# Kernel optimization log

Measured on AMD Instinct MI355X. Metric: run time of the kernel, lower is better.

The kernel has to match this reference:

```python
import jax, jax.numpy as jnp
import numpy as np

HID = 4096
H = 32
DK = 128
DV = 128
QKV = H * DK * 2 + H * DV  # 12288
EPS = 1e-06


def setup_inputs() -> dict:
    key = jax.random.key(0)
    ks = jax.random.split(key, 12)
    s = 0.02
    return {
        "hidden_states": jax.random.normal(ks[0], (1, 1, HID), jnp.float32),
        "delta_state": jax.random.normal(ks[1], (1, H, DV, DK), jnp.float32) * 0.1,
        "conv_state": jax.random.normal(ks[2], (1, QKV, 1, 3), jnp.float32),
        "W_qkv": jax.random.normal(ks[3], (QKV, HID), jnp.float32) * s,
        "W_z": jax.random.normal(ks[4], (H * DV, HID), jnp.float32) * s,
        "W_a": jax.random.normal(ks[5], (H, HID), jnp.float32) * s,
        "W_b": jax.random.normal(ks[6], (H, HID), jnp.float32) * s,
        "W_out": jax.random.normal(ks[7], (HID, H * DV), jnp.float32) * s,
        "conv_w": jax.random.normal(ks[8], (1, QKV, 1, 4), jnp.float32) * 0.01,
        "A_log": jnp.zeros((H,), jnp.float32),
        "dt_bias": jnp.zeros((H,), jnp.float32),
        "rms_weight": jnp.ones((DV,), jnp.float32),
    }


def reference(hidden_states, delta_state, conv_state, W_qkv, W_z, W_a, W_b,
              W_out, conv_w, A_log, dt_bias, rms_weight):
    hs = hidden_states[0, 0]                       # [HID]
    qkv = W_qkv @ hs                               # [QKV]
    z = W_z @ hs                                   # [H*DV]
    a = W_a @ hs                                   # [H]
    b = W_b @ hs                                   # [H]

    # manual causal conv1d decode step
    cs = conv_state[0, :, 0, :]                    # [QKV, 3]
    w = conv_w[0, :, 0, :]                         # [QKV, 4]
    conv_out = (w[:, :3] * cs).sum(-1) + w[:, 3] * qkv
    new_conv_state = jnp.concatenate([cs[:, 1:], qkv[:, None]], axis=-1)[None, :, None, :]

    qkv_act = jax.nn.silu(conv_out)
    q = qkv_act[: H * DK].reshape(H, DK)
    k = qkv_act[H * DK: 2 * H * DK].reshape(H, DK)
    v = qkv_act[2 * H * DK:].reshape(H, DV)

    # L2 normalize q, k over head dim (eps inside rsqrt), then scale q
    q = q * jax.lax.rsqrt(jnp.sum(q * q, axis=-1, keepdims=True) + 1e-06)
    k = k * jax.lax.rsqrt(jnp.sum(k * k, axis=-1, keepdims=True) + 1e-06)
    q = q * (1.0 / np.sqrt(DK))

    beta = jax.nn.sigmoid(b)                       # [H]
    gate = -jnp.exp(A_log) * jax.nn.softplus(a + dt_bias)  # [H]

    # delta-rule state update (transposed storage [H, DV, DK])
    S = delta_state[0]
    S = jnp.exp(gate)[:, None, None] * S
    retrieved = jnp.einsum('hvk,hk->hv', S, k)
    delta = beta[:, None] * (v - retrieved)
    S = S + jnp.einsum('hv,hk->hvk', delta, k)
    out = jnp.einsum('hvk,hk->hv', S, q)           # [H, DV]

    # GatedRMSNorm: RMSNorm(x) * weight * silu(z); layer_norm([x,-x]) == x/sqrt(mean(x^2)+eps)
    var = jnp.mean(out * out, axis=-1, keepdims=True)
    normed = out * jax.lax.rsqrt(var + EPS) * rms_weight
    out = normed * jax.nn.silu(z.reshape(H, DV))

    result = (W_out @ out.reshape(H * DV)).reshape(1, 1, HID)
    return result, S[None], new_conv_state
```

## Files before the change

kernel.cpp:

```cpp
#include <hip/hip_runtime.h>
#include <math.h>

#define HID 4096
#define NH 32
#define DK 128
#define DV 128
#define NQKV 12288
#define ROWS1 16448

#define OUT_S_OFF 4096
#define OUT_CONV_OFF 528384

#define WS_Z_OFF 12288
#define WS_A_OFF 16384
#define WS_B_OFF 16416
#define WS_G_OFF 16448

__device__ __forceinline__ float wave_reduce_sum(float x) {
#pragma unroll
  for (int off = 32; off > 0; off >>= 1) x += __shfl_xor(x, off, 64);
  return x;
}

__global__ __launch_bounds__(256) void k_matvec_in(
    const float* __restrict__ hs,
    const float* __restrict__ Wqkv, const float* __restrict__ Wz,
    const float* __restrict__ Wa, const float* __restrict__ Wb,
    float* __restrict__ ws) {
  const int wave = threadIdx.x >> 6, lane = threadIdx.x & 63;
  const int row = blockIdx.x * 4 + wave;
  const float* W;
  int r;
  if (row < NQKV) { W = Wqkv; r = row; }
  else if (row < NQKV + HID) { W = Wz; r = row - NQKV; }
  else if (row < NQKV + HID + NH) { W = Wa; r = row - (NQKV + HID); }
  else { W = Wb; r = row - (NQKV + HID + NH); }
  const float4* __restrict__ Wr = (const float4*)(W + (size_t)r * HID);
  const float4* __restrict__ h4 = (const float4*)hs;
  float acc = 0.f;
#pragma unroll
  for (int j = 0; j < 16; ++j) {
    const float4 w = Wr[lane + j * 64];
    const float4 h = h4[lane + j * 64];
    acc += w.x * h.x + w.y * h.y + w.z * h.z + w.w * h.w;
  }
  acc = wave_reduce_sum(acc);
  if (lane == 0) ws[row] = acc;
}

__global__ __launch_bounds__(256) void k_head(
    const float* __restrict__ delta_state, const float* __restrict__ conv_state,
    const float* __restrict__ conv_w, const float* __restrict__ A_log,
    const float* __restrict__ dt_bias, const float* __restrict__ rms_w,
    float* __restrict__ ws, float* __restrict__ dout) {
  const int h = blockIdx.x, t = threadIdx.x;
  __shared__ float S[DV * DK];
  __shared__ float qn[DK], kn[DK], va[DV], dl[DV], ov[DV];
  __shared__ float sc[4];
  __shared__ float s_eg, s_beta, s_kq;
  const float* __restrict__ qkv = ws;

  for (int idx = t; idx < 3 * 128; idx += 256) {
    const int seg = idx >> 7, li = idx & 127;
    const int row = seg * 4096 + h * 128 + li;
    const float c0 = conv_state[row * 3 + 0];
    const float c1 = conv_state[row * 3 + 1];
    const float c2 = conv_state[row * 3 + 2];
    const float w0 = conv_w[row * 4 + 0], w1 = conv_w[row * 4 + 1];
    const float w2 = conv_w[row * 4 + 2], w3 = conv_w[row * 4 + 3];
    const float x = qkv[row];
    const float co = w0 * c0 + w1 * c1 + w2 * c2 + w3 * x;
    const float act = co / (1.f + expf(-co));
    dout[OUT_CONV_OFF + row * 3 + 0] = c1;
    dout[OUT_CONV_OFF + row * 3 + 1] = c2;
    dout[OUT_CONV_OFF + row * 3 + 2] = x;
    if (seg == 0) qn[li] = act;
    else if (seg == 1) kn[li] = act;
    else va[li] = act;
  }
  __syncthreads();

  if (t < 64) {
    const float q0 = qn[t], q1 = qn[t + 64];
    const float k0 = kn[t], k1 = kn[t + 64];
    float sq = q0 * q0 + q1 * q1;
    float sk = k0 * k0 + k1 * k1;
    float dq = q0 * k0 + q1 * k1;
#pragma unroll
    for (int off = 32; off > 0; off >>= 1) {
      sq += __shfl_xor(sq, off, 64);
      sk += __shfl_xor(sk, off, 64);
      dq += __shfl_xor(dq, off, 64);
    }
    if (t == 0) {
      const float rq = rsqrtf(sq + 1e-6f) * 0.08838834764831845f;
      const float rk = rsqrtf(sk + 1e-6f);
      sc[0] = rq; sc[1] = rk;
      s_kq = dq * rq * rk;
      const float aa = ws[WS_A_OFF + h] + dt_bias[h];
      const float gate = -expf(A_log[h]) * log1pf(expf(aa));
      s_eg = expf(gate);
      const float bb = ws[WS_B_OFF + h];
      s_beta = 1.f / (1.f + expf(-bb));
    }
  }
  __syncthreads();
  if (t < 128) { qn[t] *= sc[0]; kn[t] *= sc[1]; }

  const float4* __restrict__ Sg = (const float4*)(delta_state + (size_t)h * (DV * DK));
  float4* Sl = (float4*)S;
#pragma unroll
  for (int j = 0; j < 16; ++j) Sl[j * 256 + t] = Sg[j * 256 + t];
  __syncthreads();

  const int v = t >> 1, half = t & 1;
  const float* Srow = S + v * 128 + half * 64;
  const float* kh = kn + half * 64;
  const float* qh = qn + half * 64;
  float r1 = 0.f, r2 = 0.f;
#pragma unroll
  for (int j = 0; j < 64; ++j) {
    const int jj = (j + t) & 63;
    const float s = Srow[jj];
    r1 += s * kh[jj];
    r2 += s * qh[jj];
  }
  r1 += __shfl_xor(r1, 1, 64);
  r2 += __shfl_xor(r2, 1, 64);
  const float eg = s_eg;
  const float dv_ = s_beta * (va[v] - eg * r1);
  const float o = eg * r2 + dv_ * s_kq;
  if (half == 0) { dl[v] = dv_; ov[v] = o; }
  __syncthreads();

  float4* So = (float4*)(dout + OUT_S_OFF + (size_t)h * (DV * DK));
#pragma unroll
  for (int j = 0; j < 16; ++j) {
    const int fi = j * 256 + t;
    const int vv = fi >> 5;
    const int kk = (fi & 31) << 2;
    const float4 s = Sl[fi];
    const float d = dl[vv];
    float4 rr;
    rr.x = eg * s.x + d * kn[kk + 0];
    rr.y = eg * s.y + d * kn[kk + 1];
    rr.z = eg * s.z + d * kn[kk + 2];
    rr.w = eg * s.w + d * kn[kk + 3];
    So[fi] = rr;
  }

  if (t < 64) {
    const float o0 = ov[t], o1 = ov[t + 64];
    float ss = o0 * o0 + o1 * o1;
#pragma unroll
    for (int off = 32; off > 0; off >>= 1) ss += __shfl_xor(ss, off, 64);
    if (t == 0) sc[3] = rsqrtf(ss * (1.f / 128.f) + 1e-6f);
  }
  __syncthreads();
  if (t < 128) {
    const float zv = ws[WS_Z_OFF + h * 128 + t];
    const float g = ov[t] * sc[3] * rms_w[t] * (zv / (1.f + expf(-zv)));
    ws[WS_G_OFF + h * 128 + t] = g;
  }
}

__global__ __launch_bounds__(256) void k_matvec_out(
    const float* __restrict__ Wout, const float* __restrict__ ws,
    float* __restrict__ dout) {
  const int wave = threadIdx.x >> 6, lane = threadIdx.x & 63;
  const int row = blockIdx.x * 4 + wave;
  const float4* __restrict__ Wr = (const float4*)(Wout + (size_t)row * HID);
  const float4* __restrict__ g4 = (const float4*)(ws + WS_G_OFF);
  float acc = 0.f;
#pragma unroll
  for (int j = 0; j < 16; ++j) {
    const float4 w = Wr[lane + j * 64];
    const float4 g = g4[lane + j * 64];
    acc += w.x * g.x + w.y * g.y + w.z * g.z + w.w * g.w;
  }
  acc = wave_reduce_sum(acc);
  if (lane == 0) dout[row] = acc;
}

extern "C" void kernel_launch(void* const* d_in, const int* in_sizes, int n_in,
                              void* d_out, int out_size, void* d_ws, size_t ws_size,
                              hipStream_t stream) {
  const float* hs         = (const float*)d_in[0];
  const float* delta_state= (const float*)d_in[1];
  const float* conv_state = (const float*)d_in[2];
  const float* Wqkv       = (const float*)d_in[3];
  const float* Wz         = (const float*)d_in[4];
  const float* Wa         = (const float*)d_in[5];
  const float* Wb         = (const float*)d_in[6];
  const float* Wout       = (const float*)d_in[7];
  const float* conv_w     = (const float*)d_in[8];
  const float* A_log      = (const float*)d_in[9];
  const float* dt_bias    = (const float*)d_in[10];
  const float* rms_w      = (const float*)d_in[11];
  float* ws  = (float*)d_ws;
  float* out = (float*)d_out;

  k_matvec_in<<<ROWS1 / 4, 256, 0, stream>>>(hs, Wqkv, Wz, Wa, Wb, ws);
  k_head<<<NH, 256, 0, stream>>>(delta_state, conv_state, conv_w, A_log,
                                 dt_bias, rms_w, ws, out);
  k_matvec_out<<<HID / 4, 256, 0, stream>>>(Wout, ws, out);
}
```

Baseline: 71.99 us.

## Split delta-state update across 1024 blocks and move gated norm into output matvec

The per-head state kernel, previously 32 blocks each staging a 64KB state slice through LDS, becomes 1024 blocks. Each wave handles one value row directly from global memory with float2 loads and wave reductions. The conv-state shift is written by the input matvec. RMS-norm and the SiLU gate are recomputed redundantly in every output-matvec block from raw outputs in LDS. Weight loads use nontemporal hints and expf becomes __expf; the trade-off is repeated per-block normalization work and q/k conv recomputation in every state block.

```diff
diff --git a/kernel.cpp b/kernel.cpp
--- a/kernel.cpp
+++ b/kernel.cpp
@@ -14,19 +14,26 @@
 #define WS_Z_OFF 12288
 #define WS_A_OFF 16384
 #define WS_B_OFF 16416
-#define WS_G_OFF 16448
+#define WS_O_OFF 16448
+
+typedef float f32x4 __attribute__((ext_vector_type(4)));
 
 __device__ __forceinline__ float wave_reduce_sum(float x) {
 #pragma unroll
   for (int off = 32; off > 0; off >>= 1) x += __shfl_xor(x, off, 64);
   return x;
+}
+
+__device__ __forceinline__ float silu_f(float x) {
+  return x / (1.f + __expf(-x));
 }
 
 __global__ __launch_bounds__(256) void k_matvec_in(
     const float* __restrict__ hs,
     const float* __restrict__ Wqkv, const float* __restrict__ Wz,
     const float* __restrict__ Wa, const float* __restrict__ Wb,
-    float* __restrict__ ws) {
+    const float* __restrict__ conv_state,
+    float* __restrict__ ws, float* __restrict__ dout) {
   const int wave = threadIdx.x >> 6, lane = threadIdx.x & 63;
   const int row = blockIdx.x * 4 + wave;
   const float* W;
@@ -35,48 +42,65 @@
   else if (row < NQKV + HID) { W = Wz; r = row - NQKV; }
   else if (row < NQKV + HID + NH) { W = Wa; r = row - (NQKV + HID); }
   else { W = Wb; r = row - (NQKV + HID + NH); }
-  const float4* __restrict__ Wr = (const float4*)(W + (size_t)r * HID);
-  const float4* __restrict__ h4 = (const float4*)hs;
+  const f32x4* __restrict__ Wr = (const f32x4*)(W + (size_t)r * HID);
+  const f32x4* __restrict__ h4 = (const f32x4*)hs;
   float acc = 0.f;
 #pragma unroll
   for (int j = 0; j < 16; ++j) {
-    const float4 w = Wr[lane + j * 64];
-    const float4 h = h4[lane + j * 64];
+    const f32x4 w = __builtin_nontemporal_load(&Wr[lane + j * 64]);
+    const f32x4 h = h4[lane + j * 64];
     acc += w.x * h.x + w.y * h.y + w.z * h.z + w.w * h.w;
   }
   acc = wave_reduce_sum(acc);
-  if (lane == 0) ws[row] = acc;
-}
-
-__global__ __launch_bounds__(256) void k_head(
+  if (lane == 0) {
+    ws[row] = acc;
+    if (row < NQKV) {
+      dout[OUT_CONV_OFF + row * 3 + 0] = conv_state[row * 3 + 1];
+      dout[OUT_CONV_OFF + row * 3 + 1] = conv_state[row * 3 + 2];
+      dout[OUT_CONV_OFF + row * 3 + 2] = acc;
+    }
+  }
+}
+
+__global__ __launch_bounds__(256) void k_state(
     const float* __restrict__ delta_state, const float* __restrict__ conv_state,
     const float* __restrict__ conv_w, const float* __restrict__ A_log,
-    const float* __restrict__ dt_bias, const float* __restrict__ rms_w,
+    const float* __restrict__ dt_bias,
     float* __restrict__ ws, float* __restrict__ dout) {
-  const int h = blockIdx.x, t = threadIdx.x;
-  __shared__ float S[DV * DK];
-  __shared__ float qn[DK], kn[DK], va[DV], dl[DV], ov[DV];
-  __shared__ float sc[4];
-  __shared__ float s_eg, s_beta, s_kq;
-  const float* __restrict__ qkv = ws;
-
-  for (int idx = t; idx < 3 * 128; idx += 256) {
-    const int seg = idx >> 7, li = idx & 127;
+  const int bid = blockIdx.x;
+  const int h = bid >> 5;
+  const int vbase = (bid & 31) * 4;
+  const int t = threadIdx.x;
+  __shared__ __align__(16) float qn[DK];
+  __shared__ __align__(16) float kn[DK];
+  __shared__ float va4[4];
+  __shared__ float s_eg, s_beta, s_kq, s_rq, s_rk;
+
+  {
+    const int seg = t >> 7, li = t & 127;
     const int row = seg * 4096 + h * 128 + li;
     const float c0 = conv_state[row * 3 + 0];
     const float c1 = conv_state[row * 3 + 1];
     const float c2 = conv_state[row * 3 + 2];
     const float w0 = conv_w[row * 4 + 0], w1 = conv_w[row * 4 + 1];
     const float w2 = conv_w[row * 4 + 2], w3 = conv_w[row * 4 + 3];
-    const float x = qkv[row];
-    const float co = w0 * c0 + w1 * c1 + w2 * c2 + w3 * x;
-    const float act = co / (1.f + expf(-co));
-    dout[OUT_CONV_OFF + row * 3 + 0] = c1;
-    dout[OUT_CONV_OFF + row * 3 + 1] = c2;
-    dout[OUT_CONV_OFF + row * 3 + 2] = x;
-    if (seg == 0) qn[li] = act;
-    else if (seg == 1) kn[li] = act;
-    else va[li] = act;
+    const float co = w0 * c0 + w1 * c1 + w2 * c2 + w3 * ws[row];
+    const float act = silu_f(co);
+    if (seg == 0) qn[li] = act; else kn[li] = act;
+  }
+  if (t < 4) {
+    const int row = 2 * 4096 + h * 128 + vbase + t;
+    const float c0 = conv_state[row * 3 + 0];
+    const float c1 = conv_state[row * 3 + 1];
+    const float c2 = conv_state[row * 3 + 2];
+    const float w0 = conv_w[row * 4 + 0], w1 = conv_w[row * 4 + 1];
+    const float w2 = conv_w[row * 4 + 2], w3 = conv_w[row * 4 + 3];
+    va4[t] = silu_f(w0 * c0 + w1 * c1 + w2 * c2 + w3 * ws[row]);
+  }
+  if (t == 4) {
+    const float aa = ws[WS_A_OFF + h] + dt_bias[h];
+    s_eg = __expf(-__expf(A_log[h]) * log1pf(__expf(aa)));
+    s_beta = 1.f / (1.f + __expf(-ws[WS_B_OFF + h]));
   }
   __syncthreads();
 
@@ -95,88 +119,75 @@
     if (t == 0) {
       const float rq = rsqrtf(sq + 1e-6f) * 0.08838834764831845f;
       const float rk = rsqrtf(sk + 1e-6f);
-      sc[0] = rq; sc[1] = rk;
+      s_rq = rq; s_rk = rk;
       s_kq = dq * rq * rk;
-      const float aa = ws[WS_A_OFF + h] + dt_bias[h];
-      const float gate = -expf(A_log[h]) * log1pf(expf(aa));
-      s_eg = expf(gate);
-      const float bb = ws[WS_B_OFF + h];
-      s_beta = 1.f / (1.f + expf(-bb));
-    }
-  }
-  __syncthreads();
-  if (t < 128) { qn[t] *= sc[0]; kn[t] *= sc[1]; }
-
-  const float4* __restrict__ Sg = (const float4*)(delta_state + (size_t)h * (DV * DK));
-  float4* Sl = (float4*)S;
-#pragma unroll
-  for (int j = 0; j < 16; ++j) Sl[j * 256 + t] = Sg[j * 256 + t];
-  __syncthreads();
-
-  const int v = t >> 1, half = t & 1;
-  const float* Srow = S + v * 128 + half * 64;
-  const float* kh = kn + half * 64;
-  const float* qh = qn + half * 64;
-  float r1 = 0.f, r2 = 0.f;
-#pragma unroll
-  for (int j = 0; j < 64; ++j) {
-    const int jj = (j + t) & 63;
-    const float s = Srow[jj];
-    r1 += s * kh[jj];
-    r2 += s * qh[jj];
-  }
-  r1 += __shfl_xor(r1, 1, 64);
-  r2 += __shfl_xor(r2, 1, 64);
+    }
+  }
+  __syncthreads();
+  if (t < 128) { qn[t] *= s_rq; kn[t] *= s_rk; }
+  __syncthreads();
+
+  const int w = t >> 6, lane = t & 63;
+  const int v = vbase + w;
+  const size_t roff = ((size_t)h * DV + v) * DK;
+  const float2 s2 = ((const float2*)(delta_state + roff))[lane];
+  const float2 kk = ((const float2*)kn)[lane];
+  const float2 qq = ((const float2*)qn)[lane];
+  float r1 = s2.x * kk.x + s2.y * kk.y;
+  float r2 = s2.x * qq.x + s2.y * qq.y;
+#pragma unroll
+  for (int off = 32; off > 0; off >>= 1) {
+    r1 += __shfl_xor(r1, off, 64);
+    r2 += __shfl_xor(r2, off, 64);
+  }
   const float eg = s_eg;
-  const float dv_ = s_beta * (va[v] - eg * r1);
+  const float dv_ = s_beta * (va4[w] - eg * r1);
   const float o = eg * r2 + dv_ * s_kq;
-  if (half == 0) { dl[v] = dv_; ov[v] = o; }
-  __syncthreads();
-
-  float4* So = (float4*)(dout + OUT_S_OFF + (size_t)h * (DV * DK));
+  float2 out2;
+  out2.x = eg * s2.x + dv_ * kk.x;
+  out2.y = eg * s2.y + dv_ * kk.y;
+  ((float2*)(dout + OUT_S_OFF + roff))[lane] = out2;
+  if (lane == 0) ws[WS_O_OFF + h * DV + v] = o;
+}
+
+__global__ __launch_bounds__(256) void k_matvec_out(
+    const float* __restrict__ Wout, const float* __restrict__ rms_w,
+    float* __restrict__ ws, float* __restrict__ dout) {
+  __shared__ __align__(16) float g[HID];
+  __shared__ float scale[NH];
+  const int t = threadIdx.x;
+#pragma unroll
+  for (int j = 0; j < 16; ++j) g[j * 256 + t] = ws[WS_O_OFF + j * 256 + t];
+  __syncthreads();
+  if (t < 32) {
+    float ssum = 0.f;
+#pragma unroll 4
+    for (int v = 0; v < 128; ++v) {
+      const float o = g[t * 128 + ((v + t) & 127)];
+      ssum += o * o;
+    }
+    scale[t] = rsqrtf(ssum * (1.f / 128.f) + 1e-6f);
+  }
+  __syncthreads();
 #pragma unroll
   for (int j = 0; j < 16; ++j) {
-    const int fi = j * 256 + t;
-    const int vv = fi >> 5;
-    const int kk = (fi & 31) << 2;
-    const float4 s = Sl[fi];
-    const float d = dl[vv];
-    float4 rr;
-    rr.x = eg * s.x + d * kn[kk + 0];
-    rr.y = eg * s.y + d * kn[kk + 1];
-    rr.z = eg * s.z + d * kn[kk + 2];
-    rr.w = eg * s.w + d * kn[kk + 3];
-    So[fi] = rr;
-  }
-
-  if (t < 64) {
-    const float o0 = ov[t], o1 = ov[t + 64];
-    float ss = o0 * o0 + o1 * o1;
-#pragma unroll
-    for (int off = 32; off > 0; off >>= 1) ss += __shfl_xor(ss, off, 64);
-    if (t == 0) sc[3] = rsqrtf(ss * (1.f / 128.f) + 1e-6f);
-  }
-  __syncthreads();
-  if (t < 128) {
-    const float zv = ws[WS_Z_OFF + h * 128 + t];
-    const float g = ov[t] * sc[3] * rms_w[t] * (zv / (1.f + expf(-zv)));
-    ws[WS_G_OFF + h * 128 + t] = g;
-  }
-}
-
-__global__ __launch_bounds__(256) void k_matvec_out(
-    const float* __restrict__ Wout, const float* __restrict__ ws,
-    float* __restrict__ dout) {
-  const int wave = threadIdx.x >> 6, lane = threadIdx.x & 63;
+    const int idx = j * 256 + t;
+    const int hh = idx >> 7, vv = idx & 127;
+    const float zv = ws[WS_Z_OFF + idx];
+    g[idx] = g[idx] * scale[hh] * rms_w[vv] * silu_f(zv);
+  }
+  __syncthreads();
+
+  const int wave = t >> 6, lane = t & 63;
   const int row = blockIdx.x * 4 + wave;
-  const float4* __restrict__ Wr = (const float4*)(Wout + (size_t)row * HID);
-  const float4* __restrict__ g4 = (const float4*)(ws + WS_G_OFF);
+  const f32x4* __restrict__ Wr = (const f32x4*)(Wout + (size_t)row * HID);
+  const f32x4* __restrict__ g4 = (const f32x4*)g;
   float acc = 0.f;
 #pragma unroll
   for (int j = 0; j < 16; ++j) {
-    const float4 w = Wr[lane + j * 64];
-    const float4 g = g4[lane + j * 64];
-    acc += w.x * g.x + w.y * g.y + w.z * g.z + w.w * g.w;
+    const f32x4 w = __builtin_nontemporal_load(&Wr[lane + j * 64]);
+    const f32x4 gg = g4[lane + j * 64];
+    acc += w.x * gg.x + w.y * gg.y + w.z * gg.z + w.w * gg.w;
   }
   acc = wave_reduce_sum(acc);
   if (lane == 0) dout[row] = acc;
@@ -200,8 +211,9 @@
   float* ws  = (float*)d_ws;
   float* out = (float*)d_out;
 
-  k_matvec_in<<<ROWS1 / 4, 256, 0, stream>>>(hs, Wqkv, Wz, Wa, Wb, ws);
-  k_head<<<NH, 256, 0, stream>>>(delta_state, conv_state, conv_w, A_log,
-                                 dt_bias, rms_w, ws, out);
-  k_matvec_out<<<HID / 4, 256, 0, stream>>>(Wout, ws, out);
-}
+  k_matvec_in<<<ROWS1 / 4, 256, 0, stream>>>(hs, Wqkv, Wz, Wa, Wb, conv_state,
+                                             ws, out);
+  k_state<<<NH * 32, 256, 0, stream>>>(delta_state, conv_state, conv_w, A_log,
+                                       dt_bias, ws, out);
+  k_matvec_out<<<HID / 4, 256, 0, stream>>>(Wout, rms_w, ws, out);
+}
```

Measured after the change: 65.41 us. -9.1%, faster.
